# Kernel tuning notes

Hardware: AMD Instinct MI355X
Metric: run time of the kernel (lower is better)

The kernel has to match this reference:

```python
import jax, jax.numpy as jnp
import numpy as np

B = 2048
NQ = 4
N_LAYERS = 3


def _conv(x, w, b):
    # NCHW conv, 3x3, SAME padding (padding=1 in torch)
    y = jax.lax.conv_general_dilated(x, w, (1, 1), 'SAME',
                                     dimension_numbers=('NCHW', 'OIHW', 'NCHW'))
    return y + b[None, :, None, None]


def _apply_1q(state, U, w):
    # state: (B,2,2,2,2) complex64; U: (2,2) shared or (B,2,2) batched
    s = jnp.moveaxis(state, w + 1, -1)
    if U.ndim == 2:
        s = jnp.einsum('ji,b...i->b...j', U, s)
    else:
        s = jnp.einsum('bji,b...i->b...j', U, s)
    return jnp.moveaxis(s, -1, w + 1)


def _apply_cnot(state, c, t):
    s = jnp.moveaxis(state, (c + 1, t + 1), (-2, -1))
    s = jnp.stack([s[..., 0, :], s[..., 1, ::-1]], axis=-2)  # flip target where control=1
    return jnp.moveaxis(s, (-2, -1), (c + 1, t + 1))


def _quantum(angles, weights):
    # angles: (B,4) float32; weights: (3,4,3) float32 -> (B,4) PauliZ expvals
    b = angles.shape[0]
    state = jnp.zeros((b, 2 ** NQ), jnp.complex64).at[:, 0].set(1.0)
    state = state.reshape((b,) + (2,) * NQ)
    # AngleEmbedding: RX(angles[:,w]) on wire w (batched gates)
    for w in range(NQ):
        c = jnp.cos(angles[:, w] / 2).astype(jnp.complex64)
        s = (-1j) * jnp.sin(angles[:, w] / 2).astype(jnp.complex64)
        U = jnp.stack([jnp.stack([c, s], -1), jnp.stack([s, c], -1)], -2)  # (B,2,2)
        state = _apply_1q(state, U, w)
    # StronglyEntanglingLayers: Rot per wire, then CNOT ring with range r=(l%(NQ-1))+1
    for l in range(N_LAYERS):
        for w in range(NQ):
            phi, theta, omega = weights[l, w, 0], weights[l, w, 1], weights[l, w, 2]
            ct = jnp.cos(theta / 2).astype(jnp.complex64)
            st = jnp.sin(theta / 2).astype(jnp.complex64)
            a = (phi + omega) / 2
            d = (phi - omega) / 2
            U = jnp.stack([
                jnp.stack([jnp.exp(-1j * a) * ct, -jnp.exp(1j * d) * st]),
                jnp.stack([jnp.exp(-1j * d) * st, jnp.exp(1j * a) * ct]),
            ])
            state = _apply_1q(state, U, w)
        r = (l % (NQ - 1)) + 1
        for w in range(NQ):
            state = _apply_cnot(state, w, (w + r) % NQ)
    probs = state.real ** 2 + state.imag ** 2  # (B,2,2,2,2) float32
    evs = []
    for w in range(NQ):
        m = jnp.moveaxis(probs, w + 1, 1).reshape(b, 2, -1).sum(-1)
        evs.append(m[:, 0] - m[:, 1])
    return jnp.stack(evs, axis=1)  # (B,4)


def setup_inputs() -> dict:
    key = jax.random.key(0)
    ks = jax.random.split(key, 16)
    f = jnp.float32
    return {
        'x': jax.random.normal(ks[0], (B, 3, 32, 32), f),
        'conv1_w': jax.random.normal(ks[1], (16, 3, 3, 3), f) * 0.1,
        'conv1_b': jnp.zeros((16,), f),
        'conv2_w': jax.random.normal(ks[2], (8, 16, 3, 3), f) * 0.1,
        'conv2_b': jnp.zeros((8,), f),
        'fc_w': jax.random.normal(ks[3], (4, 8 * 32 * 32), f) * 0.01,
        'fc_b': jnp.zeros((4,), f),
        'q_weights': jax.random.normal(ks[4], (N_LAYERS, NQ, 3), f),
        'fc2_w': jax.random.normal(ks[5], (8 * 32 * 32, 4), f) * 0.1,
        'fc2_b': jnp.zeros((8 * 32 * 32,), f),
        'dconv1_w': jax.random.normal(ks[6], (16, 8, 3, 3), f) * 0.1,
        'dconv1_b': jnp.zeros((16,), f),
        'dconv2_w': jax.random.normal(ks[7], (3, 16, 3, 3), f) * 0.1,
        'dconv2_b': jnp.zeros((3,), f),
    }


def reference(x, conv1_w, conv1_b, conv2_w, conv2_b, fc_w, fc_b, q_weights,
              fc2_w, fc2_b, dconv1_w, dconv1_b, dconv2_w, dconv2_b):
    h = jax.nn.relu(_conv(x, conv1_w, conv1_b))
    h = jax.nn.relu(_conv(h, conv2_w, conv2_b))
    h = h.reshape(h.shape[0], -1)                 # (B, 8192)
    ang = h @ fc_w.T + fc_b                        # (B, 4)
    q = _quantum(ang, q_weights)                   # (B, 4) batched quantum sim
    h = q @ fc2_w.T + fc2_b                        # (B, 8192)
    h = h.reshape(-1, 8, 32, 32)
    h = jax.nn.relu(_conv(h, dconv1_w, dconv1_b))
    return jax.nn.sigmoid(_conv(h, dconv2_w, dconv2_b))  # (B,3,32,32)
```

## Files before the change

kernel.cpp:

```cpp
#include <hip/hip_runtime.h>
#include <math.h>

#define T 1024
#define PS 1156
#define OFF_B   (3 * PS)
#define OFF_ROT (11 * PS)
#define OFF_ANG (OFF_ROT + 96)
#define OFF_Q   (OFF_ANG + 4)
#define OFF_RED (OFF_Q + 4)
#define LDS_FLOATS (OFF_RED + 64)

#define ZSZ (4 * 5 * 1024 * 4)

template <int NIC, int NOC, int WSTR>
__device__ __forceinline__ void conv_acc(const float* __restrict__ ib,
                                         const float* __restrict__ wg,
                                         float* __restrict__ acc) {
#pragma unroll 2
    for (int ic = 0; ic < NIC; ++ic) {
        float v[9];
#pragma unroll
        for (int ky = 0; ky < 3; ++ky)
#pragma unroll
            for (int kx = 0; kx < 3; ++kx)
                v[ky * 3 + kx] = ib[ic * PS + ky * 34 + kx];
#pragma unroll
        for (int oc = 0; oc < NOC; ++oc) {
            const float* wp = wg + oc * WSTR + ic * 9;
#pragma unroll
            for (int k = 0; k < 9; ++k)
                acc[oc] = fmaf(wp[k], v[k], acc[oc]);
        }
    }
}

__global__ __launch_bounds__(T) void prep_z_kernel(
    const float* __restrict__ f2w, const float* __restrict__ f2b,
    const float* __restrict__ d1w, const float* __restrict__ d1b,
    float* __restrict__ ws) {
    __shared__ float F[8 * PS];
    const int tid = threadIdx.x;
    const int j = blockIdx.x;
    const int py = tid >> 5, px = tid & 31;
    const int wbase = py * 34 + px;
    const int ibase = (py + 1) * 34 + (px + 1);

    for (int i = tid; i < 8 * PS; i += T) F[i] = 0.f;
    __syncthreads();
#pragma unroll
    for (int c = 0; c < 8; ++c) {
        const int idx = c * 1024 + tid;
        F[c * PS + ibase] = (j < 4) ? f2w[idx * 4 + j] : f2b[idx];
    }
    __syncthreads();
    float a1[16];
#pragma unroll
    for (int oc = 0; oc < 16; ++oc) a1[oc] = (j == 4) ? d1b[oc] : 0.f;
    conv_acc<8, 16, 72>(F + wbase, d1w, a1);
#pragma unroll
    for (int g = 0; g < 4; ++g) {
        float4 v = make_float4(a1[4 * g], a1[4 * g + 1], a1[4 * g + 2], a1[4 * g + 3]);
        *reinterpret_cast<float4*>(ws + ((g * 5 + j) * 1024 + tid) * 4) = v;
    }
}

__global__ __launch_bounds__(T) void prep_fcwt_kernel(
    const float* __restrict__ fcw, float* __restrict__ fcwT) {
    const int i = blockIdx.x * T + threadIdx.x;
#pragma unroll
    for (int o = 0; o < 4; ++o)
        fcwT[i * 4 + o] = fcw[o * 8192 + i];
}

__global__ __launch_bounds__(T, 8) void fused_kernel(
    const float* __restrict__ x,
    const float* __restrict__ c1w, const float* __restrict__ c1b,
    const float* __restrict__ c2w, const float* __restrict__ c2b,
    const float* __restrict__ fcb,
    const float* __restrict__ qw,
    const float* __restrict__ d2w, const float* __restrict__ d2b,
    const float* __restrict__ ws,
    float* __restrict__ out) {
    __shared__ float lds[LDS_FLOATS];
    float* A   = lds;
    float* Bf  = lds + OFF_B;
    float* ROT = lds + OFF_ROT;
    const float* fcwT = ws + ZSZ;

    const int tid = threadIdx.x;
    const int b   = blockIdx.x;
    const int py  = tid >> 5, px = tid & 31;
    const int wbase = py * 34 + px;
    const int ibase = (py + 1) * 34 + (px + 1);

    for (int i = tid; i < LDS_FLOATS; i += T) lds[i] = 0.f;
    __syncthreads();

    if (tid < 12) {
        float phi = qw[tid * 3 + 0], theta = qw[tid * 3 + 1], omega = qw[tid * 3 + 2];
        float a = 0.5f * (phi + omega), d = 0.5f * (phi - omega);
        float st, ct; sincosf(0.5f * theta, &st, &ct);
        float sa, ca; sincosf(a, &sa, &ca);
        float sd, cd; sincosf(d, &sd, &cd);
        float* o = ROT + tid * 8;
        o[0] = ct * ca;  o[1] = -ct * sa;
        o[2] = -st * cd; o[3] = -st * sd;
        o[4] = st * cd;  o[5] = -st * sd;
        o[6] = ct * ca;  o[7] = ct * sa;
    }

    const float* xb = x + b * 3072;
#pragma unroll
    for (int k = 0; k < 3; ++k) {
        int i = tid + k * T;
        int c = i >> 10, p = i & 1023;
        A[c * PS + ((p >> 5) + 1) * 34 + (p & 31) + 1] = xb[i];
    }
    __syncthreads();

    float acc2[8];
#pragma unroll
    for (int oc = 0; oc < 8; ++oc) acc2[oc] = c2b[oc];
    float part[4] = {0.f, 0.f, 0.f, 0.f};

    {
        float a1[8];
#pragma unroll
        for (int oc = 0; oc < 8; ++oc) a1[oc] = c1b[oc];
        conv_acc<3, 8, 27>(A + wbase, c1w, a1);
#pragma unroll
        for (int oc = 0; oc < 8; ++oc) Bf[oc * PS + ibase] = fmaxf(a1[oc], 0.f);
    }
    __syncthreads();
    conv_acc<8, 8, 144>(Bf + wbase, c2w, acc2);
    __syncthreads();
    {
        float a1[8];
#pragma unroll
        for (int oc = 0; oc < 8; ++oc) a1[oc] = c1b[8 + oc];
        conv_acc<3, 8, 27>(A + wbase, c1w + 8 * 27, a1);
#pragma unroll
        for (int oc = 0; oc < 8; ++oc) Bf[oc * PS + ibase] = fmaxf(a1[oc], 0.f);
    }
    __syncthreads();
    conv_acc<8, 8, 144>(Bf + wbase, c2w + 8 * 9, acc2);
#pragma unroll
    for (int oc = 0; oc < 8; ++oc) {
        const float h = fmaxf(acc2[oc], 0.f);
        const float4 wv = *reinterpret_cast<const float4*>(fcwT + (oc * 1024 + tid) * 4);
        part[0] = fmaf(h, wv.x, part[0]);
        part[1] = fmaf(h, wv.y, part[1]);
        part[2] = fmaf(h, wv.z, part[2]);
        part[3] = fmaf(h, wv.w, part[3]);
    }

#pragma unroll
    for (int off = 32; off; off >>= 1)
#pragma unroll
        for (int o = 0; o < 4; ++o)
            part[o] += __shfl_down(part[o], off);
    if ((tid & 63) == 0) {
        int wid = tid >> 6;
#pragma unroll
        for (int o = 0; o < 4; ++o) lds[OFF_RED + wid * 4 + o] = part[o];
    }
    __syncthreads();
    if (tid == 0) {
#pragma unroll
        for (int o = 0; o < 4; ++o) {
            float s = fcb[o];
            for (int w = 0; w < 16; ++w) s += lds[OFF_RED + w * 4 + o];
            lds[OFF_ANG + o] = s;
        }
    }
    __syncthreads();

    if (tid < 64) {
        const int s = tid & 15;
        float re = (s == 0) ? 1.f : 0.f, im = 0.f;
#pragma unroll
        for (int w = 0; w < 4; ++w) {
            float a = lds[OFF_ANG + w] * 0.5f;
            float sn, c; sincosf(a, &sn, &c);
            int stride = 1 << (3 - w);
            float pr = __shfl_xor(re, stride);
            float pi = __shfl_xor(im, stride);
            float nre = c * re + sn * pi;
            float nim = c * im - sn * pr;
            re = nre; im = nim;
        }
#pragma unroll
        for (int l = 0; l < 3; ++l) {
#pragma unroll
            for (int w = 0; w < 4; ++w) {
                const float* U = ROT + (l * 4 + w) * 8;
                int stride = 1 << (3 - w);
                bool bit = (s & stride) != 0;
                float pr = __shfl_xor(re, stride);
                float pi = __shfl_xor(im, stride);
                float cAr = bit ? U[6] : U[0], cAi = bit ? U[7] : U[1];
                float cBr = bit ? U[4] : U[2], cBi = bit ? U[5] : U[3];
                float nre = cAr * re - cAi * im + cBr * pr - cBi * pi;
                float nim = cAr * im + cAi * re + cBr * pi + cBi * pr;
                re = nre; im = nim;
            }
            const int r = (l % 3) + 1;
#pragma unroll
            for (int w = 0; w < 4; ++w) {
                int cs = 1 << (3 - w);
                int ts = 1 << (3 - ((w + r) & 3));
                float pr = __shfl_xor(re, ts);
                float pi = __shfl_xor(im, ts);
                if (s & cs) { re = pr; im = pi; }
            }
        }
        float pprob = re * re + im * im;
        float ev[4];
#pragma unroll
        for (int w = 0; w < 4; ++w)
            ev[w] = (s & (1 << (3 - w))) ? -pprob : pprob;
#pragma unroll
        for (int m = 1; m <= 8; m <<= 1)
#pragma unroll
            for (int w = 0; w < 4; ++w)
                ev[w] += __shfl_xor(ev[w], m);
        if (tid == 0) {
#pragma unroll
            for (int w = 0; w < 4; ++w) lds[OFF_Q + w] = ev[w];
        }
    }
    __syncthreads();

    const float qv[5] = {lds[OFF_Q + 0], lds[OFF_Q + 1],
                         lds[OFF_Q + 2], lds[OFF_Q + 3], 1.f};

    float acc3[3];
#pragma unroll
    for (int oc = 0; oc < 3; ++oc) acc3[oc] = d2b[oc];

#pragma unroll
    for (int h = 0; h < 2; ++h) {
#pragma unroll
        for (int gg = 0; gg < 2; ++gg) {
            const int g = h * 2 + gg;
            float4 a = make_float4(0.f, 0.f, 0.f, 0.f);
#pragma unroll
            for (int j = 0; j < 5; ++j) {
                const float4 zv = *reinterpret_cast<const float4*>(
                    ws + ((g * 5 + j) * 1024 + tid) * 4);
                a.x = fmaf(qv[j], zv.x, a.x);
                a.y = fmaf(qv[j], zv.y, a.y);
                a.z = fmaf(qv[j], zv.z, a.z);
                a.w = fmaf(qv[j], zv.w, a.w);
            }
            Bf[(gg * 4 + 0) * PS + ibase] = fmaxf(a.x, 0.f);
            Bf[(gg * 4 + 1) * PS + ibase] = fmaxf(a.y, 0.f);
            Bf[(gg * 4 + 2) * PS + ibase] = fmaxf(a.z, 0.f);
            Bf[(gg * 4 + 3) * PS + ibase] = fmaxf(a.w, 0.f);
        }
        __syncthreads();
        conv_acc<8, 3, 144>(Bf + wbase, d2w + h * 72, acc3);
        if (h == 0) __syncthreads();
    }

    {
        float* ob = out + b * 3072 + tid;
#pragma unroll
        for (int oc = 0; oc < 3; ++oc)
            ob[oc * 1024] = 1.f / (1.f + expf(-acc3[oc]));
    }
}

extern "C" void kernel_launch(void* const* d_in, const int* in_sizes, int n_in,
                              void* d_out, int out_size, void* d_ws, size_t ws_size,
                              hipStream_t stream) {
    const float* x   = (const float*)d_in[0];
    const float* c1w = (const float*)d_in[1];
    const float* c1b = (const float*)d_in[2];
    const float* c2w = (const float*)d_in[3];
    const float* c2b = (const float*)d_in[4];
    const float* fcw = (const float*)d_in[5];
    const float* fcb = (const float*)d_in[6];
    const float* qw  = (const float*)d_in[7];
    const float* f2w = (const float*)d_in[8];
    const float* f2b = (const float*)d_in[9];
    const float* d1w = (const float*)d_in[10];
    const float* d1b = (const float*)d_in[11];
    const float* d2w = (const float*)d_in[12];
    const float* d2b = (const float*)d_in[13];
    float* out = (float*)d_out;
    float* ws  = (float*)d_ws;

    prep_z_kernel<<<5, T, 0, stream>>>(f2w, f2b, d1w, d1b, ws);
    prep_fcwt_kernel<<<8, T, 0, stream>>>(fcw, ws + ZSZ);
    fused_kernel<<<2048, T, 0, stream>>>(
        x, c1w, c1b, c2w, c2b, fcb, qw, d2w, d2b, ws, out);
}
```

Measured before the change: 181.5 us.

## Interleave channels as float4 in LDS for vectorized conv loads

Changes the shared-memory layout from channel-planar floats to channel-interleaved float4 (4 channels per element), so each conv tap reads four channels with one 128-bit LDS load. The input image, the conv1 intermediate and the decoder intermediate all use this packed layout, and a new conv_q4 routine consumes it. This is meant to cut the number of LDS load instructions in the conv inner loops. In exchange there are 128-bit LDS accesses with a 16-byte per-lane stride, which may hit bank conflicts, and the input buffer gains a padded fourth channel.

```diff
diff --git a/kernel.cpp b/kernel.cpp
--- a/kernel.cpp
+++ b/kernel.cpp
@@ -3,12 +3,7 @@
 
 #define T 1024
 #define PS 1156
-#define OFF_B   (3 * PS)
-#define OFF_ROT (11 * PS)
-#define OFF_ANG (OFF_ROT + 96)
-#define OFF_Q   (OFF_ANG + 4)
-#define OFF_RED (OFF_Q + 4)
-#define LDS_FLOATS (OFF_RED + 64)
+#define PS4 1156
 
 #define ZSZ (4 * 5 * 1024 * 4)
 
@@ -30,6 +25,30 @@
 #pragma unroll
             for (int k = 0; k < 9; ++k)
                 acc[oc] = fmaf(wp[k], v[k], acc[oc]);
+        }
+    }
+}
+
+template <int NCH, int NOC, int WSTR>
+__device__ __forceinline__ void conv_q4(const float4* __restrict__ ib,
+                                        const float* __restrict__ wg,
+                                        float* __restrict__ acc) {
+#pragma unroll
+    for (int ky = 0; ky < 3; ++ky) {
+        const float4 r0 = ib[ky * 34 + 0];
+        const float4 r1 = ib[ky * 34 + 1];
+        const float4 r2 = ib[ky * 34 + 2];
+#pragma unroll
+        for (int oc = 0; oc < NOC; ++oc) {
+            const float* wp = wg + oc * WSTR + ky * 3;
+            float s = acc[oc];
+            s = fmaf(wp[0],  r0.x, s); s = fmaf(wp[1],  r1.x, s); s = fmaf(wp[2],  r2.x, s);
+            s = fmaf(wp[9],  r0.y, s); s = fmaf(wp[10], r1.y, s); s = fmaf(wp[11], r2.y, s);
+            s = fmaf(wp[18], r0.z, s); s = fmaf(wp[19], r1.z, s); s = fmaf(wp[20], r2.z, s);
+            if (NCH == 4) {
+                s = fmaf(wp[27], r0.w, s); s = fmaf(wp[28], r1.w, s); s = fmaf(wp[29], r2.w, s);
+            }
+            acc[oc] = s;
         }
     }
 }
@@ -81,10 +100,10 @@
     const float* __restrict__ d2w, const float* __restrict__ d2b,
     const float* __restrict__ ws,
     float* __restrict__ out) {
-    __shared__ float lds[LDS_FLOATS];
-    float* A   = lds;
-    float* Bf  = lds + OFF_B;
-    float* ROT = lds + OFF_ROT;
+    __shared__ float4 XQ[PS4];
+    __shared__ float4 BQ[2 * PS4];
+    __shared__ float  SM[168];
+    float* ROT = SM;
     const float* fcwT = ws + ZSZ;
 
     const int tid = threadIdx.x;
@@ -93,7 +112,10 @@
     const int wbase = py * 34 + px;
     const int ibase = (py + 1) * 34 + (px + 1);
 
-    for (int i = tid; i < LDS_FLOATS; i += T) lds[i] = 0.f;
+    const float4 z4 = make_float4(0.f, 0.f, 0.f, 0.f);
+    for (int i = tid; i < PS4; i += T) XQ[i] = z4;
+    for (int i = tid; i < 2 * PS4; i += T) BQ[i] = z4;
+    if (tid < 168) SM[tid] = 0.f;
     __syncthreads();
 
     if (tid < 12) {
@@ -109,12 +131,9 @@
         o[6] = ct * ca;  o[7] = ct * sa;
     }
 
-    const float* xb = x + b * 3072;
-#pragma unroll
-    for (int k = 0; k < 3; ++k) {
-        int i = tid + k * T;
-        int c = i >> 10, p = i & 1023;
-        A[c * PS + ((p >> 5) + 1) * 34 + (p & 31) + 1] = xb[i];
+    {
+        const float* xb = x + b * 3072;
+        XQ[ibase] = make_float4(xb[tid], xb[1024 + tid], xb[2048 + tid], 0.f);
     }
     __syncthreads();
 
@@ -123,27 +142,24 @@
     for (int oc = 0; oc < 8; ++oc) acc2[oc] = c2b[oc];
     float part[4] = {0.f, 0.f, 0.f, 0.f};
 
-    {
-        float a1[8];
-#pragma unroll
-        for (int oc = 0; oc < 8; ++oc) a1[oc] = c1b[oc];
-        conv_acc<3, 8, 27>(A + wbase, c1w, a1);
-#pragma unroll
-        for (int oc = 0; oc < 8; ++oc) Bf[oc * PS + ibase] = fmaxf(a1[oc], 0.f);
-    }
-    __syncthreads();
-    conv_acc<8, 8, 144>(Bf + wbase, c2w, acc2);
-    __syncthreads();
-    {
-        float a1[8];
-#pragma unroll
-        for (int oc = 0; oc < 8; ++oc) a1[oc] = c1b[8 + oc];
-        conv_acc<3, 8, 27>(A + wbase, c1w + 8 * 27, a1);
-#pragma unroll
-        for (int oc = 0; oc < 8; ++oc) Bf[oc * PS + ibase] = fmaxf(a1[oc], 0.f);
-    }
-    __syncthreads();
-    conv_acc<8, 8, 144>(Bf + wbase, c2w + 8 * 9, acc2);
+#pragma unroll
+    for (int h = 0; h < 2; ++h) {
+        {
+            float a1[8];
+#pragma unroll
+            for (int oc = 0; oc < 8; ++oc) a1[oc] = c1b[h * 8 + oc];
+            conv_q4<3, 8, 27>(XQ + wbase, c1w + h * 8 * 27, a1);
+            BQ[ibase]       = make_float4(fmaxf(a1[0], 0.f), fmaxf(a1[1], 0.f),
+                                          fmaxf(a1[2], 0.f), fmaxf(a1[3], 0.f));
+            BQ[PS4 + ibase] = make_float4(fmaxf(a1[4], 0.f), fmaxf(a1[5], 0.f),
+                                          fmaxf(a1[6], 0.f), fmaxf(a1[7], 0.f));
+        }
+        __syncthreads();
+        conv_q4<4, 8, 144>(BQ + wbase,       c2w + (h * 8 + 0) * 9, acc2);
+        conv_q4<4, 8, 144>(BQ + PS4 + wbase, c2w + (h * 8 + 4) * 9, acc2);
+        __syncthreads();
+    }
+
 #pragma unroll
     for (int oc = 0; oc < 8; ++oc) {
         const float h = fmaxf(acc2[oc], 0.f);
@@ -162,15 +178,15 @@
     if ((tid & 63) == 0) {
         int wid = tid >> 6;
 #pragma unroll
-        for (int o = 0; o < 4; ++o) lds[OFF_RED + wid * 4 + o] = part[o];
+        for (int o = 0; o < 4; ++o) SM[104 + wid * 4 + o] = part[o];
     }
     __syncthreads();
     if (tid == 0) {
 #pragma unroll
         for (int o = 0; o < 4; ++o) {
             float s = fcb[o];
-            for (int w = 0; w < 16; ++w) s += lds[OFF_RED + w * 4 + o];
-            lds[OFF_ANG + o] = s;
+            for (int w = 0; w < 16; ++w) s += SM[104 + w * 4 + o];
+            SM[96 + o] = s;
         }
     }
     __syncthreads();
@@ -180,7 +196,7 @@
         float re = (s == 0) ? 1.f : 0.f, im = 0.f;
 #pragma unroll
         for (int w = 0; w < 4; ++w) {
-            float a = lds[OFF_ANG + w] * 0.5f;
+            float a = SM[96 + w] * 0.5f;
             float sn, c; sincosf(a, &sn, &c);
             int stride = 1 << (3 - w);
             float pr = __shfl_xor(re, stride);
@@ -226,13 +242,12 @@
                 ev[w] += __shfl_xor(ev[w], m);
         if (tid == 0) {
 #pragma unroll
-            for (int w = 0; w < 4; ++w) lds[OFF_Q + w] = ev[w];
-        }
-    }
-    __syncthreads();
-
-    const float qv[5] = {lds[OFF_Q + 0], lds[OFF_Q + 1],
-                         lds[OFF_Q + 2], lds[OFF_Q + 3], 1.f};
+            for (int w = 0; w < 4; ++w) SM[100 + w] = ev[w];
+        }
+    }
+    __syncthreads();
+
+    const float qv[5] = {SM[100], SM[101], SM[102], SM[103], 1.f};
 
     float acc3[3];
 #pragma unroll
@@ -243,7 +258,7 @@
 #pragma unroll
         for (int gg = 0; gg < 2; ++gg) {
             const int g = h * 2 + gg;
-            float4 a = make_float4(0.f, 0.f, 0.f, 0.f);
+            float4 a = z4;
 #pragma unroll
             for (int j = 0; j < 5; ++j) {
                 const float4 zv = *reinterpret_cast<const float4*>(
@@ -253,13 +268,12 @@
                 a.z = fmaf(qv[j], zv.z, a.z);
                 a.w = fmaf(qv[j], zv.w, a.w);
             }
-            Bf[(gg * 4 + 0) * PS + ibase] = fmaxf(a.x, 0.f);
-            Bf[(gg * 4 + 1) * PS + ibase] = fmaxf(a.y, 0.f);
-            Bf[(gg * 4 + 2) * PS + ibase] = fmaxf(a.z, 0.f);
-            Bf[(gg * 4 + 3) * PS + ibase] = fmaxf(a.w, 0.f);
+            BQ[gg * PS4 + ibase] = make_float4(fmaxf(a.x, 0.f), fmaxf(a.y, 0.f),
+                                               fmaxf(a.z, 0.f), fmaxf(a.w, 0.f));
         }
         __syncthreads();
-        conv_acc<8, 3, 144>(Bf + wbase, d2w + h * 72, acc3);
+        conv_q4<4, 3, 144>(BQ + wbase,       d2w + (h * 8 + 0) * 9, acc3);
+        conv_q4<4, 3, 144>(BQ + PS4 + wbase, d2w + (h * 8 + 4) * 9, acc3);
         if (h == 0) __syncthreads();
     }
 
```

After: 320.5 us. +76.5%, slower.
